# Kernel tuning notes

Measured on AMD Instinct MI355X. Metric: run time of the kernel, lower is better.

The kernel has to match this reference:

```python
import jax, jax.numpy as jnp
import numpy as np

NEPOCHS = 100  # matches nepochs in init_kwargs


def lstm_cell(x, h, c, W_ih, W_hh, b_ih, b_hh):
    # PyTorch LSTM gate order: i, f, g, o
    gates = x @ W_ih.T + b_ih + h @ W_hh.T + b_hh  # (B, 4H)
    i, f, g, o = jnp.split(gates, 4, axis=-1)
    c_new = jax.nn.sigmoid(f) * c + jax.nn.sigmoid(i) * jnp.tanh(g)
    h_new = jax.nn.sigmoid(o) * jnp.tanh(c_new)
    return h_new, c_new


def setup_inputs() -> dict:
    key = jax.random.key(0)
    T, B, V, H, C = 400, 256, 128, 512, 64
    ks = jax.random.split(key, 8)
    s = 0.05
    return {
        "X": jax.random.normal(ks[0], (T, B, V), dtype=jnp.float32),
        "noise": jax.random.uniform(ks[1], (T, B, C), dtype=jnp.float32),
        "W_ih": jax.random.normal(ks[2], (4 * H, V + C), dtype=jnp.float32) * s,
        "W_hh": jax.random.normal(ks[3], (4 * H, H), dtype=jnp.float32) * s,
        "b_ih": jnp.zeros((4 * H,), jnp.float32),
        "b_hh": jnp.zeros((4 * H,), jnp.float32),
        "W_out": jax.random.normal(ks[4], (C, H), dtype=jnp.float32) * s,
        "b_out": jnp.zeros((C,), jnp.float32),
        "W_ctrl": jax.random.normal(ks[5], (C, H + C + 1), dtype=jnp.float32) * s,
        "b_ctrl": jnp.zeros((C,), jnp.float32),
        "epoch": 5,
    }


def reference(X, noise, W_ih, W_hh, b_ih, b_hh, W_out, b_out, W_ctrl, b_ctrl, epoch):
    T, B, V = X.shape
    C = W_out.shape[0]
    H = W_hh.shape[1]
    sg = jax.lax.stop_gradient
    # epsilon schedule: exp(-linspace(0, 7, nepochs))[epoch]  (training mode)
    eps = jnp.exp(-jnp.linspace(0.0, 7.0, NEPOCHS))[epoch]

    def step(carry, xs):
        h, c, y_bar, preds, halt_pts = carry
        x_t, n_t, t = xs
        # RNN input: raw features || detached halting indicators y_bar
        rnn_in = jnp.concatenate([x_t, sg(y_bar)], axis=-1)  # (B, V+C)
        h, c = lstm_cell(rnn_in, h, c, W_ih, W_hh, b_ih, b_hh)
        y_hat = jax.nn.sigmoid(h @ W_out.T + b_out)  # (B, C)
        time_col = t * jnp.ones((B, 1), X.dtype)
        # controller input is detached
        c_in = sg(jnp.concatenate([h, y_hat, time_col], axis=-1))  # (B, H+C+1)
        probs = jax.nn.sigmoid(c_in @ W_ctrl.T + b_ctrl)
        probs = (1.0 - eps) * probs + eps * 0.05  # explore/exploit smoothing
        a_t = n_t < probs  # Bernoulli sample via supplied uniform noise, (B,C) bool
        preds = jnp.where(a_t & (preds == 0.0), y_hat, preds)
        y_bar = jnp.where(a_t & (y_bar == 0.0), 1.0, y_bar)
        halt_pts = jnp.where((halt_pts == -1.0) & a_t, t, halt_pts)
        return (h, c, y_bar, preds, halt_pts), y_hat

    carry0 = (
        jnp.zeros((B, H), X.dtype),
        jnp.zeros((B, H), X.dtype),
        jnp.zeros((B, C), X.dtype),
        jnp.zeros((B, C), X.dtype),
        -jnp.ones((B, C), X.dtype),
    )
    ts = jnp.arange(T, dtype=X.dtype)
    (h, c, y_bar, preds, halt_pts), all_y = jax.lax.scan(step, carry0, (X, noise, ts))

    # classes never halted fall back to the last prediction
    y_hat_final = jnp.where(preds == 0.0, all_y[-1], preds)  # (B, C)
    halt_pts = jnp.where(halt_pts == -1.0, jnp.asarray(T - 1, X.dtype), halt_pts)
    mean_halting_point = (1.0 + sg(halt_pts)).mean() / (T + 1)
    return y_hat_final, mean_halting_point
```

## Files before the change

kernel.cpp:

```cpp
#include <hip/hip_runtime.h>
#include <hip/hip_cooperative_groups.h>
#include <math.h>

#define TT 400
#define BBATCH 256
#define VDIM 128
#define CDIM 64
#define HDIM 512
#define NCHUNK 11
#define TSPLIT 160

namespace cg = cooperative_groups;

typedef double d4 __attribute__((ext_vector_type(4)));

__device__ __forceinline__ double sigd(double x) {
  if (x >= 0.0) { double e = exp(-x); return 1.0 / (1.0 + e); }
  double e = exp(x); return e / (1.0 + e);
}

__global__ __launch_bounds__(256) void k_init(
    float* __restrict__ wtro, const float* __restrict__ W_out,
    float* __restrict__ wtrc, const float* __restrict__ W_ctrl,
    int* __restrict__ rowlive, int* __restrict__ alive)
{
  const int i = blockIdx.x * 256 + threadIdx.x;
  if (i < HDIM * CDIM) {
    const int k = i >> 6, c = i & 63;
    wtro[i] = W_out[c * HDIM + k];
  }
  if (i < 577 * CDIM) {
    const int k = i >> 6, c = i & 63;
    wtrc[i] = W_ctrl[c * 577 + k];
  }
  if (i < BBATCH) rowlive[i] = 1;
  if (i < TT) alive[i] = 0;
}


__device__ __forceinline__ void phase1_body(
    const float* __restrict__ X, const float* __restrict__ W_ih,
    const float* __restrict__ W_hh, const float* __restrict__ b_ih,
    const float* __restrict__ b_hh, const double* __restrict__ hR,
    double* __restrict__ hW, double* __restrict__ cst,
    const double* __restrict__ ybar, int t, int cb, int rb, int tid,
    double (*aF)[2][8][66], float (*bF)[2][2][8][68])
{
  const int lane = tid & 63;
  const int wid  = tid >> 6;
  const int r0   = rb * 16;
  const int hbase = cb * 8;

  double* gsp = &aF[0][0][0][0];

  const int sA  = tid & 7;
  const int khA = (tid >> 3) & 1;
  const int rrA = tid >> 4;

  int rowm[4], colm[4];
  {
    d4 dp = {0.0, 0.0, 0.0, 0.0};
    const double ap = (lane < 16) ? (double)(lane + 1) : (lane < 32 ? 1.0 : 0.0);
    const double bp = (lane < 16) ? 1.0
                    : (lane < 32 ? 1000.0 * (double)((lane & 15) + 1) : 0.0);
    dp = __builtin_amdgcn_mfma_f64_16x16x4f64(ap, bp, dp, 0, 0, 0);
    #pragma unroll
    for (int r = 0; r < 4; ++r) {
      const int iv = (int)(dp[r] + 0.5);
      rowm[r] = ((iv % 1000) - 1) & 15;
      colm[r] = ((iv / 1000) - 1) & 15;
    }
  }

  double pa[4];
  float4 pw0, pw1;
  const int c0 = rrA, c1 = 16 + rrA;
  const int wg0 = (c0 >> 3) * HDIM + hbase + (c0 & 7);
  const int wg1 = (c1 >> 3) * HDIM + hbase + (c1 & 7);

  auto load_to = [&](int ci) {
    const int kk = ci * 64 + khA * 32 + sA * 4;
    const int rr = r0 + rrA;
    if (kk < VDIM) {
      const float4 v = *(const float4*)(X + ((size_t)t * BBATCH + rr) * VDIM + kk);
      pa[0] = v.x; pa[1] = v.y; pa[2] = v.z; pa[3] = v.w;
    } else if (t == 0) {
      pa[0] = 0.0; pa[1] = 0.0; pa[2] = 0.0; pa[3] = 0.0;
    } else if (kk < VDIM + CDIM) {
      const double2 v0 = *(const double2*)(ybar + (size_t)rr * CDIM + (kk - VDIM));
      const double2 v1 = *(const double2*)(ybar + (size_t)rr * CDIM + (kk - VDIM) + 2);
      pa[0] = v0.x; pa[1] = v0.y; pa[2] = v1.x; pa[3] = v1.y;
    } else {
      const double2 v0 = *(const double2*)(hR + (size_t)rr * HDIM + (kk - 192));
      const double2 v1 = *(const double2*)(hR + (size_t)rr * HDIM + (kk - 192) + 2);
      pa[0] = v0.x; pa[1] = v0.y; pa[2] = v1.x; pa[3] = v1.y;
    }
    pw0 = (kk < 192) ? *(const float4*)(W_ih + (size_t)wg0 * 192 + kk)
                     : *(const float4*)(W_hh + (size_t)wg0 * HDIM + (kk - 192));
    pw1 = (kk < 192) ? *(const float4*)(W_ih + (size_t)wg1 * 192 + kk)
                     : *(const float4*)(W_hh + (size_t)wg1 * HDIM + (kk - 192));
  };
  auto store_to = [&](int buf) {
    #pragma unroll
    for (int j = 0; j < 4; ++j)
      aF[buf][khA][sA][16 * j + rrA] = pa[j];
    *(float4*)&bF[buf][khA][0][sA][rrA * 4] = pw0;
    *(float4*)&bF[buf][khA][1][sA][rrA * 4] = pw1;
  };

  const int ct = wid & 1, kh = wid >> 1;
  d4 aa = {0.0, 0.0, 0.0, 0.0}, ab = aa;

  load_to(0);
  store_to(0);
  __syncthreads();

  for (int ci = 0; ci < NCHUNK; ++ci) {
    const int p = ci & 1;
    if (ci + 1 < NCHUNK) load_to(ci + 1);
    #pragma unroll
    for (int ss = 0; ss < 8; ++ss) {
      const double av = aF[p][kh][ss][lane];
      const double bv = (double)bF[p][kh][ct][ss][(lane & 15) * 4 + (lane >> 4)];
      if (ss & 1) ab = __builtin_amdgcn_mfma_f64_16x16x4f64(av, bv, ab, 0, 0, 0);
      else        aa = __builtin_amdgcn_mfma_f64_16x16x4f64(av, bv, aa, 0, 0, 0);
    }
    if (ci + 1 < NCHUNK) store_to(p ^ 1);
    __syncthreads();
  }
  const d4 acc = aa + ab;

  #pragma unroll
  for (int r = 0; r < 4; ++r)
    gsp[kh * 528 + rowm[r] * 33 + 16 * ct + colm[r]] = acc[r];
  __syncthreads();

  if (tid < 128) {
    const int jj = tid & 7, r = tid >> 3;
    const int g0 = hbase + jj;
    const double gi = gsp[r * 33 + jj]      + gsp[528 + r * 33 + jj]
                    + (double)b_ih[0 * HDIM + g0] + (double)b_hh[0 * HDIM + g0];
    const double gf = gsp[r * 33 + 8 + jj]  + gsp[528 + r * 33 + 8 + jj]
                    + (double)b_ih[1 * HDIM + g0] + (double)b_hh[1 * HDIM + g0];
    const double gg = gsp[r * 33 + 16 + jj] + gsp[528 + r * 33 + 16 + jj]
                    + (double)b_ih[2 * HDIM + g0] + (double)b_hh[2 * HDIM + g0];
    const double go = gsp[r * 33 + 24 + jj] + gsp[528 + r * 33 + 24 + jj]
                    + (double)b_ih[3 * HDIM + g0] + (double)b_hh[3 * HDIM + g0];
    const size_t oidx = (size_t)(r0 + r) * HDIM + g0;
    const double cold = (t == 0) ? 0.0 : cst[oidx];
    const double cn = sigd(gf) * cold + sigd(gi) * tanh(gg);
    const double hn = sigd(go) * tanh(cn);
    cst[oidx] = cn;
    hW[oidx]  = hn;
  }
}

__device__ __forceinline__ void phase2_body(
    const double* __restrict__ h, const float* __restrict__ wtro,
    const float* __restrict__ b_out, const float* __restrict__ wtrc,
    const float* __restrict__ b_ctrl, const float* __restrict__ noise,
    const int* __restrict__ epoch_p, double* __restrict__ ybar,
    double* __restrict__ preds, float* __restrict__ halt,
    double* __restrict__ ylast, int* __restrict__ rowlive,
    int* __restrict__ alive, int t, int b, int tid, double* sh)
{
  double* hsh = sh;
  double* p1  = hsh + HDIM;
  double* p2  = p1 + 256;
  double* ysh = p2 + 256;

  *(double2*)&hsh[2 * tid] = *(const double2*)(h + (size_t)b * HDIM + 2 * tid);
  __syncthreads();

  const int c = tid & 63, kq = tid >> 6;
  const int k0 = kq * 128;

  double s1 = 0.0, s2 = 0.0;
  #pragma unroll 8
  for (int k = k0; k < k0 + 128; ++k) {
    const double hk = hsh[k];
    s1 += hk * (double)wtro[k * 64 + c];
    s2 += hk * (double)wtrc[k * 64 + c];
  }
  p1[kq * 64 + c] = s1;
  p2[kq * 64 + c] = s2;
  __syncthreads();

  if (tid < 64)
    ysh[tid] = sigd(p1[tid] + p1[64 + tid] + p1[128 + tid] + p1[192 + tid]
                    + (double)b_out[tid]);
  __syncthreads();

  if (tid < 64) {
    double a2 = p2[tid] + p2[64 + tid] + p2[128 + tid] + p2[192 + tid];
    #pragma unroll 8
    for (int j = 0; j < CDIM; ++j)
      a2 += ysh[j] * (double)wtrc[(512 + j) * 64 + tid];
    a2 += (double)t * (double)wtrc[576 * 64 + tid] + (double)b_ctrl[tid];

    const double eps = exp(-7.0 * (double)(*epoch_p) / 99.0);
    const double pr  = (1.0 - eps) * sigd(a2) + eps * 0.05;
    const double n   = (double)noise[((size_t)t * BBATCH + b) * CDIM + tid];
    const bool   at  = n < pr;
    const double yh  = ysh[tid];
    const size_t i   = (size_t)b * CDIM + tid;

    const double pred_old = (t == 0) ? 0.0  : preds[i];
    const double ybar_old = (t == 0) ? 0.0  : ybar[i];
    const float  halt_old = (t == 0) ? -1.0f : halt[i];

    const double pred_new = (at && pred_old == 0.0) ? yh : pred_old;
    preds[i] = pred_new;
    ybar[i]  = (at && ybar_old == 0.0) ? 1.0 : ybar_old;
    halt[i]  = (halt_old == -1.0f && at) ? (float)t : halt_old;
    ylast[i] = yh;

    const unsigned long long m = __ballot(pred_new == 0.0);
    if (tid == 0) {
      rowlive[b] = (m != 0ull) ? 1 : 0;
      if (m != 0ull) atomicOr(alive + t, 1);
    }
  }
}


__global__ __launch_bounds__(256, 4) void k_phase1(
    const float* __restrict__ X, const float* __restrict__ W_ih,
    const float* __restrict__ W_hh, const float* __restrict__ b_ih,
    const float* __restrict__ b_hh, const double* __restrict__ hR,
    double* __restrict__ hW, double* __restrict__ cst,
    const double* __restrict__ ybar, const int* __restrict__ rowlive,
    const int* __restrict__ alive, int t)
{
  if (t > 0 && alive[t - 1] == 0) return;
  const int tid = threadIdx.x, lane = tid & 63;
  const int cb = blockIdx.x, rb = blockIdx.y;
  if (t > 0) {
    const unsigned long long m =
        __ballot((lane < 16) && (rowlive[rb * 16 + (lane & 15)] != 0));
    if (m == 0ull) return;
  }
  __shared__ __align__(16) double aF[2][2][8][66];
  __shared__ __align__(16) float  bF[2][2][2][8][68];
  phase1_body(X, W_ih, W_hh, b_ih, b_hh, hR, hW, cst, ybar, t, cb, rb, tid, aF, bF);
}

__global__ __launch_bounds__(512) void k_phase2_512(
    const double* __restrict__ h, const float* __restrict__ wtro,
    const float* __restrict__ b_out, const float* __restrict__ wtrc,
    const float* __restrict__ b_ctrl, const float* __restrict__ noise,
    const int* __restrict__ epoch_p, double* __restrict__ ybar,
    double* __restrict__ preds, float* __restrict__ halt,
    double* __restrict__ ylast, int* __restrict__ rowlive,
    int* __restrict__ alive, int t)
{
  const int tid = threadIdx.x;
  const int b   = blockIdx.x;
  if (t > 0 && rowlive[b] == 0) return;

  __shared__ double hsh[HDIM];
  __shared__ double p1[8][64];
  __shared__ double p2[8][64];
  __shared__ double ysh[64];

  const int c = tid & 63, kq = tid >> 6;

  double pred_old = 0.0, ybar_old = 0.0, nse = 0.0;
  float  halt_old = -1.0f;
  if (tid < 64) {
    const size_t i = (size_t)b * CDIM + tid;
    if (t > 0) {
      pred_old = preds[i];
      ybar_old = ybar[i];
      halt_old = halt[i];
    }
    nse = (double)noise[((size_t)t * BBATCH + b) * CDIM + tid];
  }

  hsh[tid] = h[(size_t)b * HDIM + tid];
  __syncthreads();

  const int k0 = kq * 64;
  double s1 = 0.0, s2 = 0.0;
  #pragma unroll 8
  for (int k = k0; k < k0 + 64; ++k) {
    const double hk = hsh[k];
    s1 += hk * (double)wtro[k * 64 + c];
    s2 += hk * (double)wtrc[k * 64 + c];
  }
  p1[kq][c] = s1;
  p2[kq][c] = s2;
  __syncthreads();

  if (tid < 64)
    ysh[tid] = sigd(p1[0][tid] + p1[1][tid] + p1[2][tid] + p1[3][tid]
                  + p1[4][tid] + p1[5][tid] + p1[6][tid] + p1[7][tid]
                  + (double)b_out[tid]);
  __syncthreads();

  {
    double s3 = 0.0;
    #pragma unroll
    for (int j = kq * 8; j < kq * 8 + 8; ++j)
      s3 += ysh[j] * (double)wtrc[(512 + j) * 64 + c];
    p1[kq][c] = s3;
  }
  __syncthreads();

  if (tid < 64) {
    double a2 = (double)t * (double)wtrc[576 * 64 + tid] + (double)b_ctrl[tid];
    #pragma unroll
    for (int q = 0; q < 8; ++q)
      a2 += p2[q][tid] + p1[q][tid];

    const double eps = exp(-7.0 * (double)(*epoch_p) / 99.0);
    const double pr  = (1.0 - eps) * sigd(a2) + eps * 0.05;
    const bool   at  = nse < pr;
    const double yh  = ysh[tid];
    const size_t i   = (size_t)b * CDIM + tid;

    const double pred_new = (at && pred_old == 0.0) ? yh : pred_old;
    preds[i] = pred_new;
    ybar[i]  = (at && ybar_old == 0.0) ? 1.0 : ybar_old;
    halt[i]  = (halt_old == -1.0f && at) ? (float)t : halt_old;
    ylast[i] = yh;

    const unsigned long long m = __ballot(pred_new == 0.0);
    if (tid == 0) {
      rowlive[b] = (m != 0ull) ? 1 : 0;
      if (m != 0ull) atomicOr(alive + t, 1);
    }
  }
}

__global__ __launch_bounds__(256) void k_phase2(
    const double* __restrict__ h, const float* __restrict__ wtro,
    const float* __restrict__ b_out, const float* __restrict__ wtrc,
    const float* __restrict__ b_ctrl, const float* __restrict__ noise,
    const int* __restrict__ epoch_p, double* __restrict__ ybar,
    double* __restrict__ preds, float* __restrict__ halt,
    double* __restrict__ ylast, int* __restrict__ rowlive,
    int* __restrict__ alive, int t)
{
  const int tid = threadIdx.x;
  const int b   = blockIdx.x;
  if (t > 0 && rowlive[b] == 0) return;
  __shared__ double sh[HDIM + 256 + 256 + 64];
  phase2_body(h, wtro, b_out, wtrc, b_ctrl, noise, epoch_p, ybar, preds, halt,
              ylast, rowlive, alive, t, b, tid, sh);
}

__global__ __launch_bounds__(256, 4) void k_tailloop(
    const float* __restrict__ X, const float* __restrict__ W_ih,
    const float* __restrict__ W_hh, const float* __restrict__ b_ih,
    const float* __restrict__ b_hh, const float* __restrict__ wtro,
    const float* __restrict__ b_out, const float* __restrict__ wtrc,
    const float* __restrict__ b_ctrl, const float* __restrict__ noise,
    const int* __restrict__ epoch_p, double* __restrict__ h0buf,
    double* __restrict__ h1buf, double* __restrict__ cst,
    double* __restrict__ ybar, double* __restrict__ preds,
    float* __restrict__ halt, double* __restrict__ ylast,
    int* __restrict__ rowlive, int* __restrict__ alive)
{
  cg::grid_group grid = cg::this_grid();
  const int tid  = threadIdx.x;
  const int lane = tid & 63;
  const int bid  = blockIdx.x;

  __shared__ __align__(16) double aF[2][2][8][66];
  __shared__ __align__(16) float  bF[2][2][2][8][68];

  for (int t = TSPLIT; t < TT; ++t) {
    if (__hip_atomic_load(&alive[t - 1], __ATOMIC_ACQUIRE,
                          __HIP_MEMORY_SCOPE_AGENT) == 0)
      return;

    const double* hR = (t & 1) ? h1buf : h0buf;
    double*       hW = (t & 1) ? h0buf : h1buf;

    const int cb = bid & 63, rb = bid >> 6;
    const unsigned long long m =
        __ballot((lane < 16) && (rowlive[rb * 16 + (lane & 15)] != 0));
    if (m != 0ull)
      phase1_body(X, W_ih, W_hh, b_ih, b_hh, hR, hW, cst, ybar,
                  t, cb, rb, tid, aF, bF);
    grid.sync();

    if (bid < BBATCH && rowlive[bid] != 0)
      phase2_body(hW, wtro, b_out, wtrc, b_ctrl, noise, epoch_p, ybar, preds,
                  halt, ylast, rowlive, alive, t, bid, tid, &aF[0][0][0][0]);
    grid.sync();
  }
}

__global__ __launch_bounds__(256) void k_final_out(
    const double* __restrict__ preds, const double* __restrict__ ylast,
    float* __restrict__ out)
{
  const int i = blockIdx.x * 256 + threadIdx.x;
  const double p = preds[i];
  out[i] = (float)(p == 0.0 ? ylast[i] : p);
}

__global__ __launch_bounds__(256) void k_final_mean(
    const float* __restrict__ halt, float* __restrict__ out)
{
  __shared__ double s[256];
  double acc = 0.0;
  for (int i = threadIdx.x; i < BBATCH * CDIM; i += 256) {
    const float hp = halt[i];
    acc += 1.0 + (hp == -1.0f ? (double)(TT - 1) : (double)hp);
  }
  s[threadIdx.x] = acc;
  __syncthreads();
  for (int off = 128; off > 0; off >>= 1) {
    if (threadIdx.x < off) s[threadIdx.x] += s[threadIdx.x + off];
    __syncthreads();
  }
  if (threadIdx.x == 0)
    out[BBATCH * CDIM] = (float)(s[0] / (double)(BBATCH * CDIM) / (double)(TT + 1));
}

extern "C" void kernel_launch(void* const* d_in, const int* in_sizes, int n_in,
                              void* d_out, int out_size, void* d_ws, size_t ws_size,
                              hipStream_t stream)
{
  const float* X      = (const float*)d_in[0];
  const float* noise  = (const float*)d_in[1];
  const float* W_ih   = (const float*)d_in[2];
  const float* W_hh   = (const float*)d_in[3];
  const float* b_ih   = (const float*)d_in[4];
  const float* b_hh   = (const float*)d_in[5];
  const float* W_out  = (const float*)d_in[6];
  const float* b_out  = (const float*)d_in[7];
  const float* W_ctrl = (const float*)d_in[8];
  const float* b_ctrl = (const float*)d_in[9];
  const int*   epoch  = (const int*)d_in[10];
  float* out = (float*)d_out;

  char* ws = (char*)d_ws;
  double* h0      = (double*)ws;
  double* h1      = h0    + (size_t)BBATCH * HDIM;
  double* cst     = h1    + (size_t)BBATCH * HDIM;
  double* ybar    = cst   + (size_t)BBATCH * HDIM;
  double* preds   = ybar  + (size_t)BBATCH * CDIM;
  double* ylast   = preds + (size_t)BBATCH * CDIM;
  float*  halt    = (float*)(ylast + (size_t)BBATCH * CDIM);
  float*  wtro    = halt + (size_t)BBATCH * CDIM;
  float*  wtrc    = wtro + (size_t)HDIM * CDIM;
  int*    rowlive = (int*)(wtrc + (size_t)577 * CDIM);
  int*    alive   = rowlive + BBATCH;

  k_init<<<145, 256, 0, stream>>>(wtro, W_out, wtrc, W_ctrl, rowlive, alive);

  for (int t = 0; t < TSPLIT; ++t) {
    const double* hR = (t & 1) ? h1 : h0;
    double*       hW = (t & 1) ? h0 : h1;
    k_phase1<<<dim3(64, 16), 256, 0, stream>>>(X, W_ih, W_hh, b_ih, b_hh,
                                               hR, hW, cst, ybar, rowlive, alive, t);
    k_phase2_512<<<BBATCH, 512, 0, stream>>>(hW, wtro, b_out, wtrc, b_ctrl, noise,
                                             epoch, ybar, preds, halt, ylast,
                                             rowlive, alive, t);
  }

  {
    void* args[] = {
      (void*)&X, (void*)&W_ih, (void*)&W_hh, (void*)&b_ih, (void*)&b_hh,
      (void*)&wtro, (void*)&b_out, (void*)&wtrc, (void*)&b_ctrl, (void*)&noise,
      (void*)&epoch, (void*)&h0, (void*)&h1, (void*)&cst, (void*)&ybar,
      (void*)&preds, (void*)&halt, (void*)&ylast, (void*)&rowlive, (void*)&alive
    };
    hipLaunchCooperativeKernel((const void*)k_tailloop, dim3(1024), dim3(256),
                               args, 0, stream);
  }

  k_final_out<<<64, 256, 0, stream>>>(preds, ylast, out);
  k_final_mean<<<1, 256, 0, stream>>>(halt, out);
}
```

Baseline: 3.548 ms.

## Add sparse live-row fast path to LSTM phase1 when few rows remain

Phase2 now counts live batch rows per step with an atomic counter and records up to eight row indices in a list. When at most eight rows remain live, phase1 skips the tiled 16-row GEMM and runs a compact per-row matvec over W_ih and W_hh. Each live row is handled by 32 blocks, so blocks no longer do full 16-row tiles for mostly dead rows. The cost is extra atomics in phase2 and uncoalesced, non-tiled weight reads in the new path. It applies only to the first TSPLIT steps, where rows may rarely drop below the threshold.

```diff
diff --git a/kernel.cpp b/kernel.cpp
--- a/kernel.cpp
+++ b/kernel.cpp
@@ -9,6 +9,7 @@
 #define HDIM 512
 #define NCHUNK 11
 #define TSPLIT 160
+#define NTHRESH 8
 
 namespace cg = cooperative_groups;
 
@@ -22,7 +23,7 @@
 __global__ __launch_bounds__(256) void k_init(
     float* __restrict__ wtro, const float* __restrict__ W_out,
     float* __restrict__ wtrc, const float* __restrict__ W_ctrl,
-    int* __restrict__ rowlive, int* __restrict__ alive)
+    int* __restrict__ rowlive, int* __restrict__ alive, int* __restrict__ nlive)
 {
   const int i = blockIdx.x * 256 + threadIdx.x;
   if (i < HDIM * CDIM) {
@@ -34,7 +35,7 @@
     wtrc[i] = W_ctrl[c * 577 + k];
   }
   if (i < BBATCH) rowlive[i] = 1;
-  if (i < TT) alive[i] = 0;
+  if (i < TT) { alive[i] = 0; nlive[i] = 0; }
 }
 
 
@@ -230,18 +231,76 @@
     const float* __restrict__ b_hh, const double* __restrict__ hR,
     double* __restrict__ hW, double* __restrict__ cst,
     const double* __restrict__ ybar, const int* __restrict__ rowlive,
-    const int* __restrict__ alive, int t)
-{
-  if (t > 0 && alive[t - 1] == 0) return;
+    const int* __restrict__ nlive, const int* __restrict__ livelist, int t)
+{
   const int tid = threadIdx.x, lane = tid & 63;
   const int cb = blockIdx.x, rb = blockIdx.y;
+  const int bid = rb * 64 + cb;
+
+  __shared__ __align__(16) double aF[2][2][8][66];
+  __shared__ __align__(16) float  bF[2][2][2][8][68];
+
   if (t > 0) {
+    const int L = nlive[t - 1];
+    if (L == 0) return;
+
+    if (L <= NTHRESH) {
+      if (bid >= 256) return;
+      const int s = bid >> 5, c = bid & 31;
+      if (s >= L) return;
+      const int r = livelist[(t - 1) * NTHRESH + s];
+
+      double* A_lds = &aF[0][0][0][0];
+      double* psum  = A_lds + 704;
+
+      for (int k = tid; k < 704; k += 256) {
+        double v;
+        if (k < VDIM)       v = (double)X[((size_t)t * BBATCH + r) * VDIM + k];
+        else if (k < 192)   v = ybar[(size_t)r * CDIM + (k - VDIM)];
+        else                v = hR[(size_t)r * HDIM + (k - 192)];
+        A_lds[k] = v;
+      }
+      __syncthreads();
+
+      {
+        const int h16 = tid & 15, q = (tid >> 4) & 3, kq = tid >> 6;
+        const int gr = q * HDIM + c * 16 + h16;
+        const int k0 = kq * 176, k1 = k0 + 176;
+        double acc = 0.0;
+        const int ihEnd = (k1 < 192) ? k1 : 192;
+        #pragma unroll 4
+        for (int k = k0; k < ihEnd; ++k)
+          acc += A_lds[k] * (double)W_ih[(size_t)gr * 192 + k];
+        const int hhBeg = (k0 > 192) ? k0 : 192;
+        #pragma unroll 4
+        for (int k = hhBeg; k < k1; ++k)
+          acc += A_lds[k] * (double)W_hh[(size_t)gr * HDIM + (k - 192)];
+        psum[kq * 64 + q * 16 + h16] = acc;
+      }
+      __syncthreads();
+
+      if (tid < 16) {
+        const int gid = c * 16 + tid;
+        double g4[4];
+        #pragma unroll
+        for (int q = 0; q < 4; ++q)
+          g4[q] = psum[q * 16 + tid] + psum[64 + q * 16 + tid]
+                + psum[128 + q * 16 + tid] + psum[192 + q * 16 + tid]
+                + (double)b_ih[q * HDIM + gid] + (double)b_hh[q * HDIM + gid];
+        const size_t oidx = (size_t)r * HDIM + gid;
+        const double cold = cst[oidx];
+        const double cn = sigd(g4[1]) * cold + sigd(g4[0]) * tanh(g4[2]);
+        const double hn = sigd(g4[3]) * tanh(cn);
+        cst[oidx] = cn;
+        hW[oidx]  = hn;
+      }
+      return;
+    }
+
     const unsigned long long m =
         __ballot((lane < 16) && (rowlive[rb * 16 + (lane & 15)] != 0));
     if (m == 0ull) return;
   }
-  __shared__ __align__(16) double aF[2][2][8][66];
-  __shared__ __align__(16) float  bF[2][2][2][8][68];
   phase1_body(X, W_ih, W_hh, b_ih, b_hh, hR, hW, cst, ybar, t, cb, rb, tid, aF, bF);
 }
 
@@ -252,7 +311,8 @@
     const int* __restrict__ epoch_p, double* __restrict__ ybar,
     double* __restrict__ preds, float* __restrict__ halt,
     double* __restrict__ ylast, int* __restrict__ rowlive,
-    int* __restrict__ alive, int t)
+    int* __restrict__ alive, int* __restrict__ nlive,
+    int* __restrict__ livelist, int t)
 {
   const int tid = threadIdx.x;
   const int b   = blockIdx.x;
@@ -328,7 +388,11 @@
     const unsigned long long m = __ballot(pred_new == 0.0);
     if (tid == 0) {
       rowlive[b] = (m != 0ull) ? 1 : 0;
-      if (m != 0ull) atomicOr(alive + t, 1);
+      if (m != 0ull) {
+        atomicOr(alive + t, 1);
+        const int slot = atomicAdd(&nlive[t], 1);
+        if (slot < NTHRESH) livelist[t * NTHRESH + slot] = b;
+      }
     }
   }
 }
@@ -439,28 +503,31 @@
   float* out = (float*)d_out;
 
   char* ws = (char*)d_ws;
-  double* h0      = (double*)ws;
-  double* h1      = h0    + (size_t)BBATCH * HDIM;
-  double* cst     = h1    + (size_t)BBATCH * HDIM;
-  double* ybar    = cst   + (size_t)BBATCH * HDIM;
-  double* preds   = ybar  + (size_t)BBATCH * CDIM;
-  double* ylast   = preds + (size_t)BBATCH * CDIM;
-  float*  halt    = (float*)(ylast + (size_t)BBATCH * CDIM);
-  float*  wtro    = halt + (size_t)BBATCH * CDIM;
-  float*  wtrc    = wtro + (size_t)HDIM * CDIM;
-  int*    rowlive = (int*)(wtrc + (size_t)577 * CDIM);
-  int*    alive   = rowlive + BBATCH;
-
-  k_init<<<145, 256, 0, stream>>>(wtro, W_out, wtrc, W_ctrl, rowlive, alive);
+  double* h0       = (double*)ws;
+  double* h1       = h0    + (size_t)BBATCH * HDIM;
+  double* cst      = h1    + (size_t)BBATCH * HDIM;
+  double* ybar     = cst   + (size_t)BBATCH * HDIM;
+  double* preds    = ybar  + (size_t)BBATCH * CDIM;
+  double* ylast    = preds + (size_t)BBATCH * CDIM;
+  float*  halt     = (float*)(ylast + (size_t)BBATCH * CDIM);
+  float*  wtro     = halt + (size_t)BBATCH * CDIM;
+  float*  wtrc     = wtro + (size_t)HDIM * CDIM;
+  int*    rowlive  = (int*)(wtrc + (size_t)577 * CDIM);
+  int*    alive    = rowlive + BBATCH;
+  int*    nlive    = alive + TT;
+  int*    livelist = nlive + TT;
+
+  k_init<<<145, 256, 0, stream>>>(wtro, W_out, wtrc, W_ctrl, rowlive, alive, nlive);
 
   for (int t = 0; t < TSPLIT; ++t) {
     const double* hR = (t & 1) ? h1 : h0;
     double*       hW = (t & 1) ? h0 : h1;
     k_phase1<<<dim3(64, 16), 256, 0, stream>>>(X, W_ih, W_hh, b_ih, b_hh,
-                                               hR, hW, cst, ybar, rowlive, alive, t);
+                                               hR, hW, cst, ybar, rowlive,
+                                               nlive, livelist, t);
     k_phase2_512<<<BBATCH, 512, 0, stream>>>(hW, wtro, b_out, wtrc, b_ctrl, noise,
                                              epoch, ybar, preds, halt, ylast,
-                                             rowlive, alive, t);
+                                             rowlive, alive, nlive, livelist, t);
   }
 
   {
```

New measurement: 3.804 ms. 1.07x slower.
